# Performance work log

Measured on AMD Instinct MI355X. Metric: run time of the kernel, lower is better.

## Reference

```python
import jax, jax.numpy as jnp
import numpy as np

VOCAB, E, VD, B, S, W = 50000, 300, 128, 32, 64, 30
NEG = 1e12


def setup_inputs() -> dict:
    key = jax.random.key(0)
    ks = jax.random.split(key, 8)
    emb_table = jax.random.normal(ks[0], (VOCAB, E), jnp.float32) * 0.02
    emb_table = emb_table.at[0].set(0.0)  # padding_idx=0 row is zeros
    W1 = jax.random.normal(ks[1], (VD, 32), jnp.float32) * (1.0 / np.sqrt(VD))
    b1 = jnp.zeros((32,), jnp.float32)
    W2 = jax.random.normal(ks[2], (2 * E, E), jnp.float32) * (1.0 / np.sqrt(2 * E))
    b2 = jnp.zeros((E,), jnp.float32)
    word_idx = jax.random.randint(ks[3], (B, S, W), 0, VOCAB, jnp.int32)
    voice_embeded = jax.random.normal(ks[4], (B, S, VD), jnp.float32)
    sent_nums = jax.random.randint(ks[5], (B,), 1, S + 1, jnp.int32)
    return {"word_idx": word_idx, "voice_embeded": voice_embeded,
            "sent_nums": sent_nums, "max_sent_nums": S,
            "emb_table": emb_table, "W1": W1, "b1": b1, "W2": W2, "b2": b2}


def reference(word_idx, voice_embeded, sent_nums, max_sent_nums, emb_table, W1, b1, W2, b2):
    # sequence mask over sentence dim: [B, S]
    m = (jnp.arange(max_sent_nums)[None, :] < sent_nums[:, None]).astype(jnp.float32)
    word_embeded = emb_table[word_idx]                     # [B, S, W, E]
    Q = voice_embeded @ W1 + b1                            # [B, S, 32]
    K = voice_embeded @ W1 + b1                            # same dense1 weights
    A = jnp.einsum('bqd,bkd->bqk', Q, K)                   # [B, S, S]
    # additive mask applied on key axis (transpose -> add mask -> transpose back)
    A = A - (1.0 - m)[:, None, :] * NEG
    A = jax.nn.softmax(A, axis=-1)                         # voice_A
    V = word_embeded.reshape(B, max_sent_nums, -1)         # [B, S, W*E]
    O = jnp.einsum('bqk,bkd->bqd', A, V)                   # [B, S, W*E]
    O = O * m[:, :, None]                                  # multiplicative mask
    O = O.reshape(B, max_sent_nums, W, E)                  # [B, S, W, E]
    O = jnp.concatenate([O, word_embeded], axis=-1)        # [B, S, W, 2E]
    O = O @ W2 + b2                                        # [B, S, W, E]
    # transpose(1,3) then transpose(2,3): [B,S,W,E] -> [B,E,S,W]
    O = jnp.transpose(O, (0, 3, 1, 2))
    return O, A
```

## Files before the change

### kernel.cpp

```cpp
#include <hip/hip_runtime.h>

#define BB 32
#define SS 64
#define WW 30
#define EE 300
#define VDD 128
#define HH 32

typedef short bf16x8 __attribute__((ext_vector_type(8)));
typedef float f32x4 __attribute__((ext_vector_type(4)));

__device__ __forceinline__ ushort f2bf(float f) {
  union { float f; unsigned u; } x; x.f = f;
  unsigned r = x.u + 0x7fffu + ((x.u >> 16) & 1u);
  return (ushort)(r >> 16);
}
__device__ __forceinline__ float bf2f(ushort u) {
  union { unsigned u; float f; } x; x.u = ((unsigned)u) << 16; return x.f;
}

__global__ __launch_bounds__(256) void k_front(
    const float* __restrict__ voice, const int* __restrict__ sent,
    const float* __restrict__ W1, const float* __restrict__ b1,
    const int* __restrict__ widx, const float* __restrict__ emb,
    const float* __restrict__ W2,
    float* __restrict__ Aout, ushort* __restrict__ web, ushort* __restrict__ w2tp) {
  __shared__ float sq[SS][33];
  int blk = blockIdx.x, t = threadIdx.x;
  if (blk < 32) {
    int b = blk;
    for (int o = t; o < SS * HH; o += 256) {
      int s = o >> 5, j = o & 31;
      const float* vrow = voice + ((size_t)b * SS + s) * VDD;
      float acc = b1[j];
      #pragma unroll 8
      for (int d = 0; d < VDD; ++d) acc += vrow[d] * W1[d * HH + j];
      sq[s][j] = acc;
    }
    __syncthreads();
    int sn = sent[b];
    int wv = t >> 6, ln = t & 63;
    for (int q = wv; q < SS; q += 4) {
      float acc = 0.f;
      #pragma unroll
      for (int j = 0; j < HH; ++j) acc += sq[q][j] * sq[ln][j];
      if (ln >= sn) acc -= 1e12f;
      float mx = acc;
      #pragma unroll
      for (int off = 32; off; off >>= 1) mx = fmaxf(mx, __shfl_xor(mx, off));
      float e = expf(acc - mx);
      float sm = e;
      #pragma unroll
      for (int off = 32; off; off >>= 1) sm += __shfl_xor(sm, off);
      Aout[((size_t)b * SS + q) * SS + ln] = e / sm;
    }
  } else if (blk < 127) {
    int g = (blk - 32) * 256 + t;
    if (g < 380 * 64) {
      int tI = g >> 6, lane = g & 63;
      int kc2 = tI / 19, ms = tI - kc2 * 19;
      int kc = kc2 >> 1, ks = kc2 & 1;
      int lg = lane >> 4, lr = lane & 15;
      int e = ms * 16 + lr;
      int kp0 = kc * 64 + ks * 32 + lg * 8;
      ushort v[8];
      #pragma unroll
      for (int j = 0; j < 8; ++j) {
        int kp = kp0 + j;
        int c = kp < 320 ? kp : kp - 20;
        bool ok = (e < EE) && (kp < 320 ? kp < 300 : kp < 620);
        v[j] = ok ? f2bf(W2[(size_t)c * EE + e]) : (ushort)0;
      }
      ushort* dst = w2tp + (size_t)g * 8;
      *(ushort4*)dst = *(ushort4*)&v[0];
      *(ushort4*)(dst + 4) = *(ushort4*)&v[4];
    }
  } else {
    int tid = (blk - 127) * 256 + t;
    if (tid < BB * SS * WW * 75) {
      int row = tid / 75, p = tid - row * 75;
      int idx = widx[row];
      float4 v = *(const float4*)(emb + (size_t)idx * EE + p * 4);
      ushort4 o;
      o.x = f2bf(v.x); o.y = f2bf(v.y); o.z = f2bf(v.z); o.w = f2bf(v.w);
      *(ushort4*)(web + (size_t)row * EE + p * 4) = o;
    }
  }
}

__global__ __launch_bounds__(256) void k_pv(
    const float* __restrict__ Aout, const ushort* __restrict__ web,
    const int* __restrict__ sent, ushort* __restrict__ obf) {
  __shared__ float svv[SS][128];
  __shared__ float sa[SS][SS];
  int nc = blockIdx.x, b = blockIdx.y, t = threadIdx.x;
  int n0 = nc * 128;
  const float4* as = (const float4*)(Aout + (size_t)b * SS * SS);
  float4* ad = (float4*)&sa[0][0];
  for (int i = t; i < SS * SS / 4; i += 256) ad[i] = as[i];
  for (int g = t; g < SS * 32; g += 256) {
    int k = g >> 5, c4 = (g & 31) << 2;
    int n = n0 + c4;
    float4 vf = {0.f, 0.f, 0.f, 0.f};
    if (n + 3 < 9000) {
      ushort4 u = *(const ushort4*)(web + ((size_t)(b * SS + k)) * 9000 + n);
      vf.x = bf2f(u.x); vf.y = bf2f(u.y); vf.z = bf2f(u.z); vf.w = bf2f(u.w);
    }
    *(float4*)&svv[k][c4] = vf;
  }
  __syncthreads();
  int sn = sent[b];
  int qb = (t >> 5) << 3;
  int nt = (t & 31) << 2;
  float acc[8][4];
  #pragma unroll
  for (int j = 0; j < 8; ++j)
    #pragma unroll
    for (int x = 0; x < 4; ++x) acc[j][x] = 0.f;
  if (qb < sn) {
    for (int k = 0; k < sn; ++k) {
      float4 v = *(const float4*)&svv[k][nt];
      #pragma unroll
      for (int j = 0; j < 8; ++j) {
        float a = sa[qb + j][k];
        acc[j][0] += a * v.x; acc[j][1] += a * v.y;
        acc[j][2] += a * v.z; acc[j][3] += a * v.w;
      }
    }
  }
  if (n0 + nt + 3 < 9000) {
    #pragma unroll
    for (int j = 0; j < 8; ++j) {
      int q = qb + j;
      bool live = q < sn;
      ushort4 o;
      o.x = f2bf(live ? acc[j][0] : 0.f);
      o.y = f2bf(live ? acc[j][1] : 0.f);
      o.z = f2bf(live ? acc[j][2] : 0.f);
      o.w = f2bf(live ? acc[j][3] : 0.f);
      *(ushort4*)(obf + ((size_t)(b * SS + q)) * 9000 + n0 + nt) = o;
    }
  }
}

__global__ __launch_bounds__(256, 4) void k_out2(
    const ushort* __restrict__ obf, const ushort* __restrict__ web,
    const ushort* __restrict__ w2tp, const float* __restrict__ b2,
    float* __restrict__ out) {
  __shared__ ushort sb[2][64][72];
  __shared__ float sb2[304];
  int blk = blockIdx.x, t = threadIdx.x;
  int wv = t >> 6, ln = t & 63;
  size_t r0 = (size_t)blk * 64;
  int bbat = blk / 30;
  int rin0 = (blk % 30) * 64;
  for (int i = t; i < 304; i += 256) sb2[i] = (i < 300) ? b2[i] : 0.f;
  f32x4 acc[5][4];
  #pragma unroll
  for (int i = 0; i < 5; ++i)
    #pragma unroll
    for (int nf = 0; nf < 4; ++nf) acc[i][nf] = (f32x4){0.f, 0.f, 0.f, 0.f};
  int rr = t >> 2, c0 = (t & 3) << 4;
  int lr = ln & 15, lg = ln >> 4;

  uint2 pr[4];
  auto LOADK = [&](int kc) {
    const ushort* src = (kc < 5) ? obf : web;
    int cb = (kc < 5 ? kc : kc - 5) * 64 + c0;
    const ushort* s = src + (r0 + rr) * 300 + cb;
    pr[0] = *(const uint2*)(s);
    pr[1] = *(const uint2*)(s + 4);
    pr[2] = *(const uint2*)(s + 8);
    pr[3] = *(const uint2*)(s + 12);
  };
  auto WRITEK = [&](int kc, int buf) {
    int cb = (kc < 5 ? kc : kc - 5) * 64 + c0;
    if (cb + 15 < 300) {
      *(uint2*)&sb[buf][rr][c0]      = pr[0];
      *(uint2*)&sb[buf][rr][c0 + 4]  = pr[1];
      *(uint2*)&sb[buf][rr][c0 + 8]  = pr[2];
      *(uint2*)&sb[buf][rr][c0 + 12] = pr[3];
    } else {
      union { uint2 u[4]; ushort s[16]; } tmp;
      tmp.u[0] = pr[0]; tmp.u[1] = pr[1]; tmp.u[2] = pr[2]; tmp.u[3] = pr[3];
      #pragma unroll
      for (int ii = 0; ii < 16; ++ii)
        sb[buf][rr][c0 + ii] = (cb + ii < 300) ? tmp.s[ii] : (ushort)0;
    }
  };

  LOADK(0);
  WRITEK(0, 0);
  __syncthreads();
  for (int kc = 0; kc < 10; ++kc) {
    int cur = kc & 1;
    if (kc < 9) LOADK(kc + 1);
    bf16x8 bfr[4][2];
    #pragma unroll
    for (int nf = 0; nf < 4; ++nf)
      #pragma unroll
      for (int ks = 0; ks < 2; ++ks)
        bfr[nf][ks] = *(const bf16x8*)&sb[cur][nf * 16 + lr][ks * 32 + lg * 8];
    #pragma unroll
    for (int i = 0; i < 5; ++i) {
      int ms = wv + 4 * i;
      if (ms < 19) {
        #pragma unroll
        for (int ks = 0; ks < 2; ++ks) {
          bf16x8 afr = *(const bf16x8*)(w2tp +
              ((size_t)((kc * 2 + ks) * 19 + ms) * 64 + ln) * 8);
          #pragma unroll
          for (int nf = 0; nf < 4; ++nf)
            acc[i][nf] = __builtin_amdgcn_mfma_f32_16x16x32_bf16(
                afr, bfr[nf][ks], acc[i][nf], 0, 0, 0);
        }
      }
    }
    if (kc < 9) WRITEK(kc + 1, cur ^ 1);
    __syncthreads();
  }
  #pragma unroll
  for (int i = 0; i < 5; ++i) {
    int ms = wv + 4 * i;
    if (ms >= 19) continue;
    #pragma unroll
    for (int nf = 0; nf < 4; ++nf) {
      int rin = rin0 + nf * 16 + lr;
      #pragma unroll
      for (int j = 0; j < 4; ++j) {
        int e = ms * 16 + lg * 4 + j;
        if (e < 300)
          out[(size_t)(bbat * 300 + e) * 1920 + rin] = acc[i][nf][j] + sb2[e];
      }
    }
  }
}

extern "C" void kernel_launch(void* const* d_in, const int* in_sizes, int n_in,
                              void* d_out, int out_size, void* d_ws, size_t ws_size,
                              hipStream_t stream) {
  const int*   widx  = (const int*)d_in[0];
  const float* voice = (const float*)d_in[1];
  const int*   sent  = (const int*)d_in[2];
  const float* emb   = (const float*)d_in[4];
  const float* W1    = (const float*)d_in[5];
  const float* b1    = (const float*)d_in[6];
  const float* W2    = (const float*)d_in[7];
  const float* b2    = (const float*)d_in[8];
  float* out  = (float*)d_out;
  float* Aout = out + (size_t)BB * EE * SS * WW;

  ushort* web  = (ushort*)d_ws;
  ushort* obf  = web + (size_t)18432000;
  ushort* w2tp = obf + (size_t)18432000;

  hipLaunchKernelGGL(k_front, dim3(18127), dim3(256), 0, stream,
                     voice, sent, W1, b1, widx, emb, W2, Aout, web, w2tp);
  hipLaunchKernelGGL(k_pv, dim3(71, BB), dim3(256), 0, stream, Aout, web, sent, obf);
  hipLaunchKernelGGL(k_out2, dim3(960), dim3(256), 0, stream, obf, web, w2tp, b2, out);
}
```

Baseline: 143.6 us.

## Rewrite attention-times-V kernel with bf16 MFMA and swizzled transposed LDS tile

Replaces the scalar FP32 A·V kernel with a bf16 MFMA version. Each block now covers 256 columns instead of 128, and the V tile is stored transposed in LDS with an XOR swizzle to avoid bank conflicts. The attention matrix is converted to bf16, which lowers its precision, and K-steps and M-tiles beyond sent_nums are skipped. The output is written as scattered 2-byte stores, and the occupancy hint on k_out2 is also removed.

After: 125.6 us. 12.6% less time.

```diff
diff --git a/kernel.cpp b/kernel.cpp
--- a/kernel.cpp
+++ b/kernel.cpp
@@ -88,62 +88,86 @@
   }
 }
 
-__global__ __launch_bounds__(256) void k_pv(
+__global__ __launch_bounds__(256) void k_pv2(
     const float* __restrict__ Aout, const ushort* __restrict__ web,
     const int* __restrict__ sent, ushort* __restrict__ obf) {
-  __shared__ float svv[SS][128];
-  __shared__ float sa[SS][SS];
+  __shared__ ushort sa[64][72];
+  __shared__ ushort vt[256][72];
   int nc = blockIdx.x, b = blockIdx.y, t = threadIdx.x;
-  int n0 = nc * 128;
-  const float4* as = (const float4*)(Aout + (size_t)b * SS * SS);
-  float4* ad = (float4*)&sa[0][0];
-  for (int i = t; i < SS * SS / 4; i += 256) ad[i] = as[i];
-  for (int g = t; g < SS * 32; g += 256) {
-    int k = g >> 5, c4 = (g & 31) << 2;
-    int n = n0 + c4;
-    float4 vf = {0.f, 0.f, 0.f, 0.f};
-    if (n + 3 < 9000) {
-      ushort4 u = *(const ushort4*)(web + ((size_t)(b * SS + k)) * 9000 + n);
-      vf.x = bf2f(u.x); vf.y = bf2f(u.y); vf.z = bf2f(u.z); vf.w = bf2f(u.w);
-    }
-    *(float4*)&svv[k][c4] = vf;
+  int n0blk = nc * 256;
+  for (int i = t; i < 64 * 16; i += 256) {
+    int q = i >> 4, c4 = (i & 15) << 2;
+    float4 f = *(const float4*)(Aout + (size_t)b * 4096 + q * 64 + c4);
+    ushort4 u; u.x = f2bf(f.x); u.y = f2bf(f.y); u.z = f2bf(f.z); u.w = f2bf(f.w);
+    *(ushort4*)&sa[q][c4] = u;
+  }
+  int kk = t >> 5, nl0 = (t & 31) << 3;
+  int swz = (t & 31) & 7;
+  for (int p = 0; p < 8; ++p) {
+    int k = p * 8 + kk;
+    int n = n0blk + nl0;
+    ushort v[8];
+    if (n + 7 < 9000) {
+      const ushort* s = web + (size_t)(b * 64 + k) * 9000 + n;
+      *(ushort4*)&v[0] = *(const ushort4*)s;
+      *(ushort4*)&v[4] = *(const ushort4*)(s + 4);
+    } else {
+      #pragma unroll
+      for (int j = 0; j < 8; ++j) v[j] = 0;
+    }
+    int c = (((k >> 3) ^ swz) << 3) + (k & 7);
+    #pragma unroll
+    for (int j = 0; j < 8; ++j) vt[nl0 + j][c] = v[j];
   }
   __syncthreads();
   int sn = sent[b];
-  int qb = (t >> 5) << 3;
-  int nt = (t & 31) << 2;
-  float acc[8][4];
-  #pragma unroll
-  for (int j = 0; j < 8; ++j)
-    #pragma unroll
-    for (int x = 0; x < 4; ++x) acc[j][x] = 0.f;
-  if (qb < sn) {
-    for (int k = 0; k < sn; ++k) {
-      float4 v = *(const float4*)&svv[k][nt];
-      #pragma unroll
-      for (int j = 0; j < 8; ++j) {
-        float a = sa[qb + j][k];
-        acc[j][0] += a * v.x; acc[j][1] += a * v.y;
-        acc[j][2] += a * v.z; acc[j][3] += a * v.w;
-      }
-    }
-  }
-  if (n0 + nt + 3 < 9000) {
-    #pragma unroll
-    for (int j = 0; j < 8; ++j) {
-      int q = qb + j;
-      bool live = q < sn;
-      ushort4 o;
-      o.x = f2bf(live ? acc[j][0] : 0.f);
-      o.y = f2bf(live ? acc[j][1] : 0.f);
-      o.z = f2bf(live ? acc[j][2] : 0.f);
-      o.w = f2bf(live ? acc[j][3] : 0.f);
-      *(ushort4*)(obf + ((size_t)(b * SS + q)) * 9000 + n0 + nt) = o;
-    }
-  }
-}
-
-__global__ __launch_bounds__(256, 4) void k_out2(
+  int wv = t >> 6, ln = t & 63, lr = ln & 15, lg = ln >> 4;
+  int nbase = wv * 64;
+  f32x4 acc[4][4];
+  #pragma unroll
+  for (int mt = 0; mt < 4; ++mt)
+    #pragma unroll
+    for (int nf = 0; nf < 4; ++nf) acc[mt][nf] = (f32x4){0.f, 0.f, 0.f, 0.f};
+  #pragma unroll
+  for (int ks = 0; ks < 2; ++ks) {
+    if (ks * 32 < sn) {
+      bf16x8 bfrag[4];
+      #pragma unroll
+      for (int nf = 0; nf < 4; ++nf) {
+        int row = nbase + nf * 16 + lr;
+        int gp = (ks * 4 + lg) ^ ((row >> 3) & 7);
+        bfrag[nf] = *(const bf16x8*)&vt[row][gp << 3];
+      }
+      #pragma unroll
+      for (int mt = 0; mt < 4; ++mt) {
+        if (mt * 16 < sn) {
+          bf16x8 afrag = *(const bf16x8*)&sa[mt * 16 + lr][ks * 32 + lg * 8];
+          #pragma unroll
+          for (int nf = 0; nf < 4; ++nf)
+            acc[mt][nf] = __builtin_amdgcn_mfma_f32_16x16x32_bf16(
+                afrag, bfrag[nf], acc[mt][nf], 0, 0, 0);
+        }
+      }
+    }
+  }
+  #pragma unroll
+  for (int mt = 0; mt < 4; ++mt) {
+    #pragma unroll
+    for (int nf = 0; nf < 4; ++nf) {
+      int n = n0blk + nbase + nf * 16 + lr;
+      if (n < 9000) {
+        #pragma unroll
+        for (int j = 0; j < 4; ++j) {
+          int q = mt * 16 + lg * 4 + j;
+          obf[(size_t)(b * 64 + q) * 9000 + n] =
+              (q < sn) ? f2bf(acc[mt][nf][j]) : (ushort)0;
+        }
+      }
+    }
+  }
+}
+
+__global__ __launch_bounds__(256) void k_out2(
     const ushort* __restrict__ obf, const ushort* __restrict__ web,
     const ushort* __restrict__ w2tp, const float* __restrict__ b2,
     float* __restrict__ out) {
@@ -256,6 +280,6 @@
 
   hipLaunchKernelGGL(k_front, dim3(18127), dim3(256), 0, stream,
                      voice, sent, W1, b1, widx, emb, W2, Aout, web, w2tp);
-  hipLaunchKernelGGL(k_pv, dim3(71, BB), dim3(256), 0, stream, Aout, web, sent, obf);
+  hipLaunchKernelGGL(k_pv2, dim3(36, BB), dim3(256), 0, stream, Aout, web, sent, obf);
   hipLaunchKernelGGL(k_out2, dim3(960), dim3(256), 0, stream, obf, web, w2tp, b2, out);
 }
```
